# Kernel tuning notes

Measured on AMD Instinct MI355X. Metric: run time of the kernel, lower is better.

## Reference

```python
import jax, jax.numpy as jnp
import numpy as np
import math

B, S, D, H = 4, 2048, 1024, 16
DK = D // H  # 64


def setup_inputs() -> dict:
    key = jax.random.key(0)
    ks = jax.random.split(key, 10)
    scale = 1.0 / math.sqrt(D)
    inp = {
        "context_sequence": jax.random.normal(ks[0], (B, S, D), dtype=jnp.float32),
        "value_sequence": jax.random.normal(ks[1], (B, S, D), dtype=jnp.float32),
        "mask": jax.random.randint(ks[2], (S, S), 0, 2, dtype=jnp.int32),
        # stacked per-head projection params: [H, D, DK] weights, [H, DK] biases
        "Wq": jax.random.uniform(ks[3], (H, D, DK), jnp.float32, -scale, scale),
        "bq": jnp.zeros((H, DK), jnp.float32),
        "Wk": jax.random.uniform(ks[4], (H, D, DK), jnp.float32, -scale, scale),
        "bk": jnp.zeros((H, DK), jnp.float32),
        "Wv": jax.random.uniform(ks[5], (H, D, DK), jnp.float32, -scale, scale),
        "bv": jnp.zeros((H, DK), jnp.float32),
        "Wo": jax.random.uniform(ks[6], (D, D), jnp.float32, -scale, scale),
        "bo": jnp.zeros((D,), jnp.float32),
    }
    return inp


def reference(context_sequence, value_sequence, mask, Wq, bq, Wk, bk, Wv, bv, Wo, bo):
    # per-head projections batched over heads: [B,H,S,DK]
    Q = jnp.einsum("bsd,hdk->bhsk", context_sequence, Wq) + bq[None, :, None, :]
    K = jnp.einsum("bsd,hdk->bhsk", context_sequence, Wk) + bk[None, :, None, :]
    V = jnp.einsum("bsd,hdk->bhsk", value_sequence, Wv) + bv[None, :, None, :]
    scores = jnp.einsum("bhsk,bhtk->bhst", Q, K) / math.sqrt(DK)
    scores = jnp.where(mask[None, None, :, :] == 1, jnp.float32(-1e9), scores)
    attn = jax.nn.softmax(scores, axis=-1)
    out = jnp.einsum("bhst,bhtk->bhsk", attn, V)  # [B,H,S,DK]
    concat = out.transpose(0, 2, 1, 3).reshape(B, S, D)  # heads concatenated
    # output projection (dropout is identity in eval mode)
    return concat @ Wo.T + bo
```

## Files before the change

### kernel.cpp

```cpp
#include <hip/hip_runtime.h>
#include <hip/hip_bf16.h>

#define DEVI __device__ __forceinline__

typedef __attribute__((ext_vector_type(8))) short bf16x8;
typedef __attribute__((ext_vector_type(4))) float f32x4;
typedef unsigned short u16;
typedef unsigned long long u64;


DEVI void async16(const void* g, const void* l) {
  __builtin_amdgcn_global_load_lds(
      (const __attribute__((address_space(1))) unsigned int*)g,
      (__attribute__((address_space(3))) unsigned int*)l, 16, 0, 0);
}

DEVI u16 f2bf(float x) {
  unsigned int u = __float_as_uint(x);
  return (u16)((u + 0x7fffu + ((u >> 16) & 1u)) >> 16);
}

DEVI float fast_exp2(float x) {
#if __has_builtin(__builtin_amdgcn_exp2f)
  return __builtin_amdgcn_exp2f(x);
#else
  return exp2f(x);
#endif
}


__global__ __launch_bounds__(256) void prep_kernel(
    const float* __restrict__ ctx, const float* __restrict__ val, const int* __restrict__ msk,
    const float* __restrict__ Wq, const float* __restrict__ Wk, const float* __restrict__ Wv,
    const float* __restrict__ Wo, const float* __restrict__ bq, const float* __restrict__ bk,
    u16* __restrict__ Xc, u16* __restrict__ Xv, u16* __restrict__ Wqt, u16* __restrict__ Wkt,
    u16* __restrict__ Wvt, u16* __restrict__ WoB, u64* __restrict__ mbits, float* __restrict__ bqk) {
  __shared__ float tile[64 * 69];
  const int blk = blockIdx.x, tid = threadIdx.x;
  if (blk < 16384) {
    const float* src = (blk < 8192) ? ctx : val;
    u16* dst = (blk < 8192) ? Xc : Xv;
    int i = (blk & 8191) * 256 + tid;
    float4 v = ((const float4*)src)[i];
    ushort4 o;
    o.x = f2bf(v.x); o.y = f2bf(v.y); o.z = f2bf(v.z); o.w = f2bf(v.w);
    ((ushort4*)dst)[i] = o;
  } else if (blk < 17408) {
    int i = (blk - 16384) * 256 + tid;
    float4 v = ((const float4*)Wo)[i];
    ushort4 o;
    o.x = f2bf(v.x); o.y = f2bf(v.y); o.z = f2bf(v.z); o.w = f2bf(v.w);
    ((ushort4*)WoB)[i] = o;
  } else if (blk < 18176) {
    int t = blk - 17408;
    int mat = t >> 8, r = t & 255, h = r >> 4, d0 = (r & 15) * 64;
    const float* Ws = (mat == 0) ? Wq : (mat == 1) ? Wk : Wv;
    u16* Wd = (mat == 0) ? Wqt : (mat == 1) ? Wkt : Wvt;
    const int dg = tid & 15, rg = tid >> 4;
#pragma unroll
    for (int i = 0; i < 4; i++) {
      int dr = rg + i * 16;
      float4 v = *(const float4*)&Ws[((size_t)(h * 1024 + d0 + dr)) * 64 + dg * 4];
      tile[dr * 69 + dg * 4 + 0] = v.x;
      tile[dr * 69 + dg * 4 + 1] = v.y;
      tile[dr * 69 + dg * 4 + 2] = v.z;
      tile[dr * 69 + dg * 4 + 3] = v.w;
    }
    __syncthreads();
#pragma unroll
    for (int i = 0; i < 4; i++) {
      int k = rg + i * 16;
      ushort4 o;
      o.x = f2bf(tile[(dg * 4 + 0) * 69 + k]);
      o.y = f2bf(tile[(dg * 4 + 1) * 69 + k]);
      o.z = f2bf(tile[(dg * 4 + 2) * 69 + k]);
      o.w = f2bf(tile[(dg * 4 + 3) * 69 + k]);
      *(ushort4*)&Wd[(size_t)(h * 64 + k) * 1024 + d0 + dg * 4] = o;
    }
  } else if (blk < 34560) {
    int gid = (blk - 18176) * 256 + tid;
    u64 bal = __ballot(msk[gid] == 1);
    if ((tid & 63) == 0) mbits[gid >> 6] = bal;
  } else {
    int i = (blk - 34560) * 256 + tid;
    bqk[i] = (i < 1024) ? bq[i] : bk[i - 1024];
  }
}


template <int MODE>
__global__ __launch_bounds__(256) void gemm_bt(const u16* __restrict__ A, const u16* __restrict__ Bt,
                                               const float* __restrict__ bias, void* __restrict__ C,
                                               int M, int N, int K, float oscale, float oscale2, int nsplit) {
  __shared__ __align__(16) u16 As[128 * 32];
  __shared__ __align__(16) u16 Bs[128 * 32];
  const int tid = threadIdx.x;
  const int w = tid >> 6, lane = tid & 63, quad = lane >> 4, lc = lane & 15;
  const int m0 = blockIdx.x * 128, n0 = blockIdx.y * 128;
  const int wrow = (w >> 1) * 64, wcol = (w & 1) * 64;
  const int srow = tid >> 2, sc = tid & 3;
  const u16* Ag = A + (size_t)(m0 + srow) * K + sc * 8;
  const u16* Bg = Bt + (size_t)(n0 + srow) * K + sc * 8;
  u16* Asw = As + w * 512;
  u16* Bsw = Bs + w * 512;

  f32x4 acc[4][4] = {};
  for (int k0 = 0; k0 < K; k0 += 32) {
    async16(Ag + k0, Asw);
    async16(Ag + k0 + (size_t)64 * K, Asw + 2048);
    async16(Bg + k0, Bsw);
    async16(Bg + k0 + (size_t)64 * K, Bsw + 2048);
    __syncthreads();
    bf16x8 af[4], bfr[4];
#pragma unroll
    for (int rt = 0; rt < 4; rt++) af[rt] = *(const bf16x8*)&As[(wrow + rt * 16 + lc) * 32 + quad * 8];
#pragma unroll
    for (int ct = 0; ct < 4; ct++) bfr[ct] = *(const bf16x8*)&Bs[(wcol + ct * 16 + lc) * 32 + quad * 8];
#pragma unroll
    for (int rt = 0; rt < 4; rt++)
#pragma unroll
      for (int ct = 0; ct < 4; ct++)
        acc[rt][ct] = __builtin_amdgcn_mfma_f32_16x16x32_bf16(af[rt], bfr[ct], acc[rt][ct], 0, 0, 0);
    __syncthreads();
  }
#pragma unroll
  for (int ct = 0; ct < 4; ct++) {
    int col = n0 + wcol + ct * 16 + lc;
    float bv = bias[col];
    float os = (MODE == 0 && col >= nsplit) ? oscale2 : oscale;
#pragma unroll
    for (int rt = 0; rt < 4; rt++) {
      if (MODE == 2) {
        int trow = m0 + wrow + rt * 16 + quad * 4;
        ushort4 pk;
        pk.x = f2bf((acc[rt][ct][0] + bv) * os);
        pk.y = f2bf((acc[rt][ct][1] + bv) * os);
        pk.z = f2bf((acc[rt][ct][2] + bv) * os);
        pk.w = f2bf((acc[rt][ct][3] + bv) * os);
        size_t off = ((size_t)(trow >> 11) * 1024 + col) * 2048 + (trow & 2047);
        *(ushort4*)((u16*)C + off) = pk;
      } else {
#pragma unroll
        for (int r = 0; r < 4; r++) {
          int row = m0 + wrow + rt * 16 + quad * 4 + r;
          float v = (acc[rt][ct][r] + bv) * os;
          if (MODE == 1) ((float*)C)[(size_t)row * N + col] = v;
          else           ((u16*)C)[(size_t)row * N + col] = f2bf(v);
        }
      }
    }
  }
}


__global__ __launch_bounds__(256) void attn_kernel(const u16* __restrict__ QK, const u16* __restrict__ Vt,
                                                   const u64* __restrict__ mbits, u16* __restrict__ AO) {
  __shared__ __align__(16) u16 Ks[2][4096];
  __shared__ __align__(16) u16 Vs[2][4096];
  __shared__ __align__(16) u16 QP[4096];
  const int S = 2048, D = 1024, QS = 2048;
  const int tid = threadIdx.x, w = tid >> 6, lane = tid & 63, quad = lane >> 4, lc = lane & 15;
  const int q0 = blockIdx.x * 64;
  const int b = blockIdx.y >> 4, h = blockIdx.y & 15;
  const size_t baseq = (size_t)b * S * QS + (size_t)h * 64;
  const size_t vbase = (size_t)blockIdx.y * 64 * S;
  const int sr = lane >> 3, gch = (lane & 7) ^ sr, lx = lc & 7;

  {
    const u16* g0 = QK + baseq + (size_t)(q0 + w * 16 + sr) * QS + gch * 8;
    async16(g0, QP + w * 1024);
    async16(g0 + (size_t)8 * QS, QP + w * 1024 + 512);
  }
  const u16* Kg0 = QK + baseq + 1024 + (size_t)(w * 16 + sr) * QS + gch * 8;
  const u16* Vg0 = Vt + vbase + (size_t)(w * 16 + sr) * S + gch * 8;
  __syncthreads();

  bf16x8 aq[2];
  {
    const int arow = w * 16 + lc;
    aq[0] = *(const bf16x8*)&QP[arow * 64 + ((quad ^ lx) << 3)];
    aq[1] = *(const bf16x8*)&QP[arow * 64 + (((4 + quad) ^ lx) << 3)];
  }

  async16(Kg0, Ks[0] + w * 1024);
  async16(Kg0 + (size_t)8 * QS, Ks[0] + w * 1024 + 512);
  async16(Vg0, Vs[0] + w * 1024);
  async16(Vg0 + (size_t)8 * S, Vs[0] + w * 1024 + 512);

  const u64* mbase = mbits + (size_t)(q0 + w * 16 + quad * 4) * (S / 64);

  bf16x8 ones;
#pragma unroll
  for (int j = 0; j < 8; j++) ones[j] = (short)0x3F80;

  f32x4 acco[4] = {};
  f32x4 accl = {};

  for (int t0 = 0; t0 < S; t0 += 64) {
    const int cur = (t0 >> 6) & 1;
    __syncthreads();
    if (t0 + 64 < S) {
      const u16* Kg = Kg0 + (size_t)(t0 + 64) * QS;
      const u16* Vg = Vg0 + (t0 + 64);
      async16(Kg, Ks[cur ^ 1] + w * 1024);
      async16(Kg + (size_t)8 * QS, Ks[cur ^ 1] + w * 1024 + 512);
      async16(Vg, Vs[cur ^ 1] + w * 1024);
      async16(Vg + (size_t)8 * S, Vs[cur ^ 1] + w * 1024 + 512);
    }
    u64 mword[4];
#pragma unroll
    for (int r = 0; r < 4; r++) mword[r] = mbase[(size_t)r * 32 + (t0 >> 6)];

    f32x4 sacc[4] = {};
#pragma unroll
    for (int ks = 0; ks < 2; ks++)
#pragma unroll
      for (int ct = 0; ct < 4; ct++) {
        bf16x8 bk = *(const bf16x8*)&Ks[cur][(ct * 16 + lc) * 64 + (((ks * 4 + quad) ^ lx) << 3)];
        sacc[ct] = __builtin_amdgcn_mfma_f32_16x16x32_bf16(aq[ks], bk, sacc[ct], 0, 0, 0);
      }

#pragma unroll
    for (int r = 0; r < 4; r++) {
      u64 wsh = mword[r] >> lc;
      unsigned int lo = (unsigned int)wsh, hi = (unsigned int)(wsh >> 32);
      float p0 = fast_exp2((lo & 1u)           ? -1e4f : sacc[0][r]);
      float p1 = fast_exp2((lo & 0x10000u)     ? -1e4f : sacc[1][r]);
      float p2 = fast_exp2((hi & 1u)           ? -1e4f : sacc[2][r]);
      float p3 = fast_exp2((hi & 0x10000u)     ? -1e4f : sacc[3][r]);
      const int q = quad * 4 + r, qx = q & 7, lch = lc >> 3;
      const int pb = w * 1024 + q * 64 + lx;
      QP[pb + (((0 + lch) ^ qx) << 3)] = (u16)(__float_as_uint(p0) >> 16);
      QP[pb + (((2 + lch) ^ qx) << 3)] = (u16)(__float_as_uint(p1) >> 16);
      QP[pb + (((4 + lch) ^ qx) << 3)] = (u16)(__float_as_uint(p2) >> 16);
      QP[pb + (((6 + lch) ^ qx) << 3)] = (u16)(__float_as_uint(p3) >> 16);
    }

#pragma unroll
    for (int ks = 0; ks < 2; ks++) {
      bf16x8 ap = *(const bf16x8*)&QP[w * 1024 + lc * 64 + (((ks * 4 + quad) ^ lx) << 3)];
#pragma unroll
      for (int ct = 0; ct < 4; ct++) {
        bf16x8 bv = *(const bf16x8*)&Vs[cur][(ct * 16 + lc) * 64 + (((ks * 4 + quad) ^ lx) << 3)];
        acco[ct] = __builtin_amdgcn_mfma_f32_16x16x32_bf16(ap, bv, acco[ct], 0, 0, 0);
      }
      accl = __builtin_amdgcn_mfma_f32_16x16x32_bf16(ap, ones, accl, 0, 0, 0);
    }
  }

#pragma unroll
  for (int r = 0; r < 4; r++) {
    float inv = 1.0f / accl[r];
    size_t row = (size_t)b * S + q0 + w * 16 + quad * 4 + r;
#pragma unroll
    for (int ct = 0; ct < 4; ct++)
      AO[row * D + h * 64 + ct * 16 + lc] = f2bf(acco[ct][r] * inv);
  }
}


extern "C" void kernel_launch(void* const* d_in, const int* in_sizes, int n_in,
                              void* d_out, int out_size, void* d_ws, size_t ws_size,
                              hipStream_t stream) {
  const int B = 4, S = 2048, D = 1024;
  const float* ctx = (const float*)d_in[0];
  const float* val = (const float*)d_in[1];
  const int*   msk = (const int*)d_in[2];
  const float* Wq  = (const float*)d_in[3];
  const float* bq  = (const float*)d_in[4];
  const float* Wk  = (const float*)d_in[5];
  const float* bk  = (const float*)d_in[6];
  const float* Wv  = (const float*)d_in[7];
  const float* bv  = (const float*)d_in[8];
  const float* Wo  = (const float*)d_in[9];
  const float* bo  = (const float*)d_in[10];
  float* out = (float*)d_out;

  char* ws = (char*)d_ws;
  size_t off = 0;
  auto alloc = [&](size_t sz) { void* p = ws + off; off += (sz + 255) & ~255ULL; return p; };
  const size_t NTOK = (size_t)B * S * D;
  u16* Xc  = (u16*)alloc(NTOK * 2);
  u16* Xv  = (u16*)alloc(NTOK * 2);
  u16* Wqt = (u16*)alloc((size_t)D * D * 2);
  u16* Wkt = (u16*)alloc((size_t)D * D * 2);
  u16* Wvt = (u16*)alloc((size_t)D * D * 2);
  u16* WoB = (u16*)alloc((size_t)D * D * 2);
  u16* QKb = (u16*)alloc(NTOK * 4);
  u16* Vtg = (u16*)alloc(NTOK * 2);
  u64* mbits = (u64*)alloc((size_t)S * S / 8);
  float* bqk = (float*)alloc(2048 * 4);
  u16* AO = Xc;
  if (off > ws_size) return;

  const float qscale = 0.125f * 1.44269504088896f;

  prep_kernel<<<34568, 256, 0, stream>>>(ctx, val, msk, Wq, Wk, Wv, Wo, bq, bk,
                                         Xc, Xv, Wqt, Wkt, Wvt, WoB, mbits, bqk);

  gemm_bt<0><<<dim3(B * S / 128, 2048 / 128), 256, 0, stream>>>(
      Xc, Wqt, bqk, QKb, B * S, 2048, D, qscale, 1.0f, 1024);
  gemm_bt<2><<<dim3(B * S / 128, D / 128), 256, 0, stream>>>(
      Xv, Wvt, bv, Vtg, B * S, D, D, 1.0f, 1.0f, D);

  attn_kernel<<<dim3(S / 64, B * 16), 256, 0, stream>>>(QKb, Vtg, mbits, AO);

  gemm_bt<1><<<dim3(B * S / 128, D / 128), 256, 0, stream>>>(
      AO, WoB, bo, out, B * S, D, D, 1.0f, 1.0f, D);
}
```

Measured before the change: 388.0 us.

## Process 128 queries per attention block and merge Q/K/V projection GEMMs

The attention kernel now gives each wave 32 query rows instead of 16, so every K/V tile staged in shared memory serves twice as many queries. This halves the global K/V traffic and the number of blocks. The mask bit layout is transposed so each tile's mask words are contiguous per key block. The QK and V projection GEMMs are merged into one launch, and the output GEMM is specialized. In exchange, each wave needs more registers for two sets of accumulators, which may lower occupancy.

```diff
diff --git a/kernel.cpp b/kernel.cpp
--- a/kernel.cpp
+++ b/kernel.cpp
@@ -80,7 +80,7 @@
   } else if (blk < 34560) {
     int gid = (blk - 18176) * 256 + tid;
     u64 bal = __ballot(msk[gid] == 1);
-    if ((tid & 63) == 0) mbits[gid >> 6] = bal;
+    if ((tid & 63) == 0) mbits[(size_t)((gid >> 6) & 31) * 2048 + (gid >> 11)] = bal;
   } else {
     int i = (blk - 34560) * 256 + tid;
     bqk[i] = (i < 1024) ? bq[i] : bk[i - 1024];
@@ -88,14 +88,193 @@
 }
 
 
-template <int MODE>
-__global__ __launch_bounds__(256) void gemm_bt(const u16* __restrict__ A, const u16* __restrict__ Bt,
-                                               const float* __restrict__ bias, void* __restrict__ C,
-                                               int M, int N, int K, float oscale, float oscale2, int nsplit) {
+__global__ __launch_bounds__(256) void qkv_gemm(const u16* __restrict__ Xc, const u16* __restrict__ Xv,
+                                                const u16* __restrict__ Wqkt, const u16* __restrict__ Wvt,
+                                                const float* __restrict__ bqk, const float* __restrict__ bvv,
+                                                u16* __restrict__ QKb, u16* __restrict__ Vtg, float qscale) {
   __shared__ __align__(16) u16 As[128 * 32];
   __shared__ __align__(16) u16 Bs[128 * 32];
   const int tid = threadIdx.x;
   const int w = tid >> 6, lane = tid & 63, quad = lane >> 4, lc = lane & 15;
+  const int K = 1024;
+  const bool isV = blockIdx.y >= 16;
+  const int m0 = blockIdx.x * 128;
+  const int n0 = (isV ? (blockIdx.y - 16) : blockIdx.y) * 128;
+  const u16* A  = isV ? Xv : Xc;
+  const u16* Bt = isV ? Wvt : Wqkt;
+  const float* bias = isV ? bvv : bqk;
+  const int wrow = (w >> 1) * 64, wcol = (w & 1) * 64;
+  const int srow = tid >> 2, sc = tid & 3;
+  const u16* Ag = A + (size_t)(m0 + srow) * K + sc * 8;
+  const u16* Bg = Bt + (size_t)(n0 + srow) * K + sc * 8;
+  u16* Asw = As + w * 512;
+  u16* Bsw = Bs + w * 512;
+
+  f32x4 acc[4][4] = {};
+  for (int k0 = 0; k0 < K; k0 += 32) {
+    async16(Ag + k0, Asw);
+    async16(Ag + k0 + (size_t)64 * K, Asw + 2048);
+    async16(Bg + k0, Bsw);
+    async16(Bg + k0 + (size_t)64 * K, Bsw + 2048);
+    __syncthreads();
+    bf16x8 af[4], bfr[4];
+#pragma unroll
+    for (int rt = 0; rt < 4; rt++) af[rt] = *(const bf16x8*)&As[(wrow + rt * 16 + lc) * 32 + quad * 8];
+#pragma unroll
+    for (int ct = 0; ct < 4; ct++) bfr[ct] = *(const bf16x8*)&Bs[(wcol + ct * 16 + lc) * 32 + quad * 8];
+#pragma unroll
+    for (int rt = 0; rt < 4; rt++)
+#pragma unroll
+      for (int ct = 0; ct < 4; ct++)
+        acc[rt][ct] = __builtin_amdgcn_mfma_f32_16x16x32_bf16(af[rt], bfr[ct], acc[rt][ct], 0, 0, 0);
+    __syncthreads();
+  }
+#pragma unroll
+  for (int ct = 0; ct < 4; ct++) {
+    int col = n0 + wcol + ct * 16 + lc;
+    float bv = bias[col];
+    float os = (!isV && col < 1024) ? qscale : 1.0f;
+#pragma unroll
+    for (int rt = 0; rt < 4; rt++) {
+      if (isV) {
+        int trow = m0 + wrow + rt * 16 + quad * 4;
+        ushort4 pk;
+        pk.x = f2bf(acc[rt][ct][0] + bv);
+        pk.y = f2bf(acc[rt][ct][1] + bv);
+        pk.z = f2bf(acc[rt][ct][2] + bv);
+        pk.w = f2bf(acc[rt][ct][3] + bv);
+        size_t off = ((size_t)(trow >> 11) * 1024 + col) * 2048 + (trow & 2047);
+        *(ushort4*)(Vtg + off) = pk;
+      } else {
+#pragma unroll
+        for (int r = 0; r < 4; r++) {
+          int row = m0 + wrow + rt * 16 + quad * 4 + r;
+          QKb[(size_t)row * 2048 + col] = f2bf((acc[rt][ct][r] + bv) * os);
+        }
+      }
+    }
+  }
+}
+
+
+__global__ __launch_bounds__(256, 4) void attn_kernel(const u16* __restrict__ QK, const u16* __restrict__ Vt,
+                                                      const u64* __restrict__ mbits, u16* __restrict__ AO) {
+  __shared__ __align__(16) u16 Ks[2][4096];
+  __shared__ __align__(16) u16 Vs[2][4096];
+  __shared__ __align__(16) u16 Ps[4096];
+  const int S = 2048, D = 1024, QS = 2048;
+  const int tid = threadIdx.x, w = tid >> 6, lane = tid & 63, quad = lane >> 4, lc = lane & 15;
+  const int q0 = blockIdx.x * 128;
+  const int b = blockIdx.y >> 4, h = blockIdx.y & 15;
+  const size_t baseq = (size_t)b * S * QS + (size_t)h * 64;
+  const size_t vbase = (size_t)blockIdx.y * 64 * S;
+  const int sr = lane >> 3, gch = (lane & 7) ^ sr, lx = lc & 7;
+  u16* Ksq = (u16*)Ks;
+
+#pragma unroll
+  for (int i = 0; i < 4; i++) {
+    const u16* g = QK + baseq + (size_t)(q0 + w * 32 + i * 8 + sr) * QS + gch * 8;
+    async16(g, Ksq + w * 2048 + i * 512);
+  }
+  const u16* Kg0 = QK + baseq + 1024 + (size_t)(w * 16 + sr) * QS + gch * 8;
+  const u16* Vg0 = Vt + vbase + (size_t)(w * 16 + sr) * S + gch * 8;
+  __syncthreads();
+
+  bf16x8 aq[2][2];
+#pragma unroll
+  for (int s = 0; s < 2; s++)
+#pragma unroll
+    for (int ks = 0; ks < 2; ks++)
+      aq[s][ks] = *(const bf16x8*)&Ksq[w * 2048 + (s * 16 + lc) * 64 + (((ks * 4 + quad) ^ lx) << 3)];
+  __syncthreads();
+
+  async16(Kg0, Ks[0] + w * 1024);
+  async16(Kg0 + (size_t)8 * QS, Ks[0] + w * 1024 + 512);
+  async16(Vg0, Vs[0] + w * 1024);
+  async16(Vg0 + (size_t)8 * S, Vs[0] + w * 1024 + 512);
+
+  const u64* mrow = mbits + (size_t)(q0 + w * 32 + quad * 4);
+
+  bf16x8 ones;
+#pragma unroll
+  for (int j = 0; j < 8; j++) ones[j] = (short)0x3F80;
+
+  f32x4 acco[2][4] = {};
+  f32x4 accl[2] = {};
+
+  for (int t0 = 0; t0 < S; t0 += 64) {
+    const int cur = (t0 >> 6) & 1;
+    __syncthreads();
+    if (t0 + 64 < S) {
+      const u16* Kg = Kg0 + (size_t)(t0 + 64) * QS;
+      const u16* Vg = Vg0 + (t0 + 64);
+      async16(Kg, Ks[cur ^ 1] + w * 1024);
+      async16(Kg + (size_t)8 * QS, Ks[cur ^ 1] + w * 1024 + 512);
+      async16(Vg, Vs[cur ^ 1] + w * 1024);
+      async16(Vg + (size_t)8 * S, Vs[cur ^ 1] + w * 1024 + 512);
+    }
+
+    f32x4 sacc[2][4] = {};
+#pragma unroll
+    for (int ks = 0; ks < 2; ks++)
+#pragma unroll
+      for (int ct = 0; ct < 4; ct++) {
+        bf16x8 bk = *(const bf16x8*)&Ks[cur][(ct * 16 + lc) * 64 + (((ks * 4 + quad) ^ lx) << 3)];
+        sacc[0][ct] = __builtin_amdgcn_mfma_f32_16x16x32_bf16(aq[0][ks], bk, sacc[0][ct], 0, 0, 0);
+        sacc[1][ct] = __builtin_amdgcn_mfma_f32_16x16x32_bf16(aq[1][ks], bk, sacc[1][ct], 0, 0, 0);
+      }
+
+#pragma unroll
+    for (int s = 0; s < 2; s++) {
+#pragma unroll
+      for (int r = 0; r < 4; r++) {
+        u64 word = mrow[(size_t)(t0 >> 6) * 2048 + s * 16 + r];
+        u64 wsh = word >> lc;
+        unsigned int lo = (unsigned int)wsh, hi = (unsigned int)(wsh >> 32);
+        float p0 = fast_exp2((lo & 1u)       ? -1e4f : sacc[s][0][r]);
+        float p1 = fast_exp2((lo & 0x10000u) ? -1e4f : sacc[s][1][r]);
+        float p2 = fast_exp2((hi & 1u)       ? -1e4f : sacc[s][2][r]);
+        float p3 = fast_exp2((hi & 0x10000u) ? -1e4f : sacc[s][3][r]);
+        const int q = quad * 4 + r, qx = q & 7, lch = lc >> 3;
+        const int pb = w * 1024 + q * 64 + lx;
+        Ps[pb + (((0 + lch) ^ qx) << 3)] = (u16)(__float_as_uint(p0) >> 16);
+        Ps[pb + (((2 + lch) ^ qx) << 3)] = (u16)(__float_as_uint(p1) >> 16);
+        Ps[pb + (((4 + lch) ^ qx) << 3)] = (u16)(__float_as_uint(p2) >> 16);
+        Ps[pb + (((6 + lch) ^ qx) << 3)] = (u16)(__float_as_uint(p3) >> 16);
+      }
+#pragma unroll
+      for (int ks = 0; ks < 2; ks++) {
+        bf16x8 ap = *(const bf16x8*)&Ps[w * 1024 + lc * 64 + (((ks * 4 + quad) ^ lx) << 3)];
+#pragma unroll
+        for (int ct = 0; ct < 4; ct++) {
+          bf16x8 bv = *(const bf16x8*)&Vs[cur][(ct * 16 + lc) * 64 + (((ks * 4 + quad) ^ lx) << 3)];
+          acco[s][ct] = __builtin_amdgcn_mfma_f32_16x16x32_bf16(ap, bv, acco[s][ct], 0, 0, 0);
+        }
+        accl[s] = __builtin_amdgcn_mfma_f32_16x16x32_bf16(ap, ones, accl[s], 0, 0, 0);
+      }
+    }
+  }
+
+#pragma unroll
+  for (int s = 0; s < 2; s++)
+#pragma unroll
+    for (int r = 0; r < 4; r++) {
+      float inv = 1.0f / accl[s][r];
+      size_t row = (size_t)b * S + q0 + w * 32 + s * 16 + quad * 4 + r;
+#pragma unroll
+      for (int ct = 0; ct < 4; ct++)
+        AO[row * D + h * 64 + ct * 16 + lc] = f2bf(acco[s][ct][r] * inv);
+    }
+}
+
+
+__global__ __launch_bounds__(256) void out_gemm(const u16* __restrict__ A, const u16* __restrict__ Bt,
+                                                const float* __restrict__ bias, float* __restrict__ C) {
+  __shared__ __align__(16) u16 As[128 * 32];
+  __shared__ __align__(16) u16 Bs[128 * 32];
+  const int tid = threadIdx.x;
+  const int w = tid >> 6, lane = tid & 63, quad = lane >> 4, lc = lane & 15;
+  const int K = 1024, N = 1024;
   const int m0 = blockIdx.x * 128, n0 = blockIdx.y * 128;
   const int wrow = (w >> 1) * 64, wcol = (w & 1) * 64;
   const int srow = tid >> 2, sc = tid & 3;
@@ -127,134 +306,13 @@
   for (int ct = 0; ct < 4; ct++) {
     int col = n0 + wcol + ct * 16 + lc;
     float bv = bias[col];
-    float os = (MODE == 0 && col >= nsplit) ? oscale2 : oscale;
-#pragma unroll
-    for (int rt = 0; rt < 4; rt++) {
-      if (MODE == 2) {
-        int trow = m0 + wrow + rt * 16 + quad * 4;
-        ushort4 pk;
-        pk.x = f2bf((acc[rt][ct][0] + bv) * os);
-        pk.y = f2bf((acc[rt][ct][1] + bv) * os);
-        pk.z = f2bf((acc[rt][ct][2] + bv) * os);
-        pk.w = f2bf((acc[rt][ct][3] + bv) * os);
-        size_t off = ((size_t)(trow >> 11) * 1024 + col) * 2048 + (trow & 2047);
-        *(ushort4*)((u16*)C + off) = pk;
-      } else {
-#pragma unroll
-        for (int r = 0; r < 4; r++) {
-          int row = m0 + wrow + rt * 16 + quad * 4 + r;
-          float v = (acc[rt][ct][r] + bv) * os;
-          if (MODE == 1) ((float*)C)[(size_t)row * N + col] = v;
-          else           ((u16*)C)[(size_t)row * N + col] = f2bf(v);
-        }
-      }
-    }
-  }
-}
-
-
-__global__ __launch_bounds__(256) void attn_kernel(const u16* __restrict__ QK, const u16* __restrict__ Vt,
-                                                   const u64* __restrict__ mbits, u16* __restrict__ AO) {
-  __shared__ __align__(16) u16 Ks[2][4096];
-  __shared__ __align__(16) u16 Vs[2][4096];
-  __shared__ __align__(16) u16 QP[4096];
-  const int S = 2048, D = 1024, QS = 2048;
-  const int tid = threadIdx.x, w = tid >> 6, lane = tid & 63, quad = lane >> 4, lc = lane & 15;
-  const int q0 = blockIdx.x * 64;
-  const int b = blockIdx.y >> 4, h = blockIdx.y & 15;
-  const size_t baseq = (size_t)b * S * QS + (size_t)h * 64;
-  const size_t vbase = (size_t)blockIdx.y * 64 * S;
-  const int sr = lane >> 3, gch = (lane & 7) ^ sr, lx = lc & 7;
-
-  {
-    const u16* g0 = QK + baseq + (size_t)(q0 + w * 16 + sr) * QS + gch * 8;
-    async16(g0, QP + w * 1024);
-    async16(g0 + (size_t)8 * QS, QP + w * 1024 + 512);
-  }
-  const u16* Kg0 = QK + baseq + 1024 + (size_t)(w * 16 + sr) * QS + gch * 8;
-  const u16* Vg0 = Vt + vbase + (size_t)(w * 16 + sr) * S + gch * 8;
-  __syncthreads();
-
-  bf16x8 aq[2];
-  {
-    const int arow = w * 16 + lc;
-    aq[0] = *(const bf16x8*)&QP[arow * 64 + ((quad ^ lx) << 3)];
-    aq[1] = *(const bf16x8*)&QP[arow * 64 + (((4 + quad) ^ lx) << 3)];
-  }
-
-  async16(Kg0, Ks[0] + w * 1024);
-  async16(Kg0 + (size_t)8 * QS, Ks[0] + w * 1024 + 512);
-  async16(Vg0, Vs[0] + w * 1024);
-  async16(Vg0 + (size_t)8 * S, Vs[0] + w * 1024 + 512);
-
-  const u64* mbase = mbits + (size_t)(q0 + w * 16 + quad * 4) * (S / 64);
-
-  bf16x8 ones;
-#pragma unroll
-  for (int j = 0; j < 8; j++) ones[j] = (short)0x3F80;
-
-  f32x4 acco[4] = {};
-  f32x4 accl = {};
-
-  for (int t0 = 0; t0 < S; t0 += 64) {
-    const int cur = (t0 >> 6) & 1;
-    __syncthreads();
-    if (t0 + 64 < S) {
-      const u16* Kg = Kg0 + (size_t)(t0 + 64) * QS;
-      const u16* Vg = Vg0 + (t0 + 64);
-      async16(Kg, Ks[cur ^ 1] + w * 1024);
-      async16(Kg + (size_t)8 * QS, Ks[cur ^ 1] + w * 1024 + 512);
-      async16(Vg, Vs[cur ^ 1] + w * 1024);
-      async16(Vg + (size_t)8 * S, Vs[cur ^ 1] + w * 1024 + 512);
-    }
-    u64 mword[4];
-#pragma unroll
-    for (int r = 0; r < 4; r++) mword[r] = mbase[(size_t)r * 32 + (t0 >> 6)];
-
-    f32x4 sacc[4] = {};
-#pragma unroll
-    for (int ks = 0; ks < 2; ks++)
-#pragma unroll
-      for (int ct = 0; ct < 4; ct++) {
-        bf16x8 bk = *(const bf16x8*)&Ks[cur][(ct * 16 + lc) * 64 + (((ks * 4 + quad) ^ lx) << 3)];
-        sacc[ct] = __builtin_amdgcn_mfma_f32_16x16x32_bf16(aq[ks], bk, sacc[ct], 0, 0, 0);
-      }
-
-#pragma unroll
-    for (int r = 0; r < 4; r++) {
-      u64 wsh = mword[r] >> lc;
-      unsigned int lo = (unsigned int)wsh, hi = (unsigned int)(wsh >> 32);
-      float p0 = fast_exp2((lo & 1u)           ? -1e4f : sacc[0][r]);
-      float p1 = fast_exp2((lo & 0x10000u)     ? -1e4f : sacc[1][r]);
-      float p2 = fast_exp2((hi & 1u)           ? -1e4f : sacc[2][r]);
-      float p3 = fast_exp2((hi & 0x10000u)     ? -1e4f : sacc[3][r]);
-      const int q = quad * 4 + r, qx = q & 7, lch = lc >> 3;
-      const int pb = w * 1024 + q * 64 + lx;
-      QP[pb + (((0 + lch) ^ qx) << 3)] = (u16)(__float_as_uint(p0) >> 16);
-      QP[pb + (((2 + lch) ^ qx) << 3)] = (u16)(__float_as_uint(p1) >> 16);
-      QP[pb + (((4 + lch) ^ qx) << 3)] = (u16)(__float_as_uint(p2) >> 16);
-      QP[pb + (((6 + lch) ^ qx) << 3)] = (u16)(__float_as_uint(p3) >> 16);
-    }
-
-#pragma unroll
-    for (int ks = 0; ks < 2; ks++) {
-      bf16x8 ap = *(const bf16x8*)&QP[w * 1024 + lc * 64 + (((ks * 4 + quad) ^ lx) << 3)];
-#pragma unroll
-      for (int ct = 0; ct < 4; ct++) {
-        bf16x8 bv = *(const bf16x8*)&Vs[cur][(ct * 16 + lc) * 64 + (((ks * 4 + quad) ^ lx) << 3)];
-        acco[ct] = __builtin_amdgcn_mfma_f32_16x16x32_bf16(ap, bv, acco[ct], 0, 0, 0);
-      }
-      accl = __builtin_amdgcn_mfma_f32_16x16x32_bf16(ap, ones, accl, 0, 0, 0);
-    }
-  }
-
-#pragma unroll
-  for (int r = 0; r < 4; r++) {
-    float inv = 1.0f / accl[r];
-    size_t row = (size_t)b * S + q0 + w * 16 + quad * 4 + r;
-#pragma unroll
-    for (int ct = 0; ct < 4; ct++)
-      AO[row * D + h * 64 + ct * 16 + lc] = f2bf(acco[ct][r] * inv);
+#pragma unroll
+    for (int rt = 0; rt < 4; rt++)
+#pragma unroll
+      for (int r = 0; r < 4; r++) {
+        int row = m0 + wrow + rt * 16 + quad * 4 + r;
+        C[(size_t)row * N + col] = acc[rt][ct][r] + bv;
+      }
   }
 }
 
@@ -298,13 +356,9 @@
   prep_kernel<<<34568, 256, 0, stream>>>(ctx, val, msk, Wq, Wk, Wv, Wo, bq, bk,
                                          Xc, Xv, Wqt, Wkt, Wvt, WoB, mbits, bqk);
 
-  gemm_bt<0><<<dim3(B * S / 128, 2048 / 128), 256, 0, stream>>>(
-      Xc, Wqt, bqk, QKb, B * S, 2048, D, qscale, 1.0f, 1024);
-  gemm_bt<2><<<dim3(B * S / 128, D / 128), 256, 0, stream>>>(
-      Xv, Wvt, bv, Vtg, B * S, D, D, 1.0f, 1.0f, D);
-
-  attn_kernel<<<dim3(S / 64, B * 16), 256, 0, stream>>>(QKb, Vtg, mbits, AO);
-
-  gemm_bt<1><<<dim3(B * S / 128, D / 128), 256, 0, stream>>>(
-      AO, WoB, bo, out, B * S, D, D, 1.0f, 1.0f, D);
-}
+  qkv_gemm<<<dim3(B * S / 128, 24), 256, 0, stream>>>(Xc, Xv, Wqt, Wvt, bqk, bv, QKb, Vtg, qscale);
+
+  attn_kernel<<<dim3(S / 128, B * 16), 256, 0, stream>>>(QKb, Vtg, mbits, AO);
+
+  out_gemm<<<dim3(B * S / 128, D / 128), 256, 0, stream>>>(AO, WoB, bo, out);
+}
```

After: 366.6 us. -5.5%, faster.
